# Performance work log

Measured on AMD Instinct MI355X. Metric: run time of the kernel, lower is better.

The kernel has to match this reference:

```python
import jax, jax.numpy as jnp
import numpy as np

B, T, C, HS = 64, 256, 2048, 128


def setup_inputs() -> dict:
    key = jax.random.key(0)
    k1, k2, k3, k4 = jax.random.split(key, 4)
    x = jax.random.normal(k1, (B, T, C), dtype=jnp.float32)
    # Dense(head_size, use_bias=False) kernels, scaled like glorot-ish init
    Wk = jax.random.normal(k2, (C, HS), dtype=jnp.float32) * (C ** -0.5)
    Wq = jax.random.normal(k3, (C, HS), dtype=jnp.float32) * (C ** -0.5)
    Wv = jax.random.normal(k4, (C, HS), dtype=jnp.float32) * (C ** -0.5)
    return {"x": x, "Wk": Wk, "Wq": Wq, "Wv": Wv}


def reference(x, Wk, Wq, Wv):
    Bn, Tn, Cn = x.shape
    k = jnp.einsum("btc,ch->bth", x, Wk)
    q = jnp.einsum("btc,ch->bth", x, Wq)
    v = jnp.einsum("btc,ch->bth", x, Wv)
    # faithful to source: scores = k @ q^T, scaled by C**-0.5 (input dim!)
    scores = jnp.einsum("bth,bsh->bts", k, q) * (Cn ** -0.5)
    causal = jnp.tril(jnp.ones((Tn, Tn), dtype=bool))  # [T, T]
    scores = jnp.where(causal, scores, -jnp.inf)
    weights = jax.nn.softmax(scores, axis=-1)
    return jnp.einsum("bts,bsh->bth", weights, v)
```

## Files before the change

kernel.cpp:

```cpp
#include <hip/hip_runtime.h>
#include <hip/hip_bf16.h>
#include <cstdint>
#include <cstddef>

#define B_  64
#define T_  256
#define C_  2048
#define HS_ 128
#define N_  384

typedef __bf16 bf16x8 __attribute__((ext_vector_type(8)));
typedef float  floatx4 __attribute__((ext_vector_type(4)));

__device__ __forceinline__ unsigned short f2bf_rne(float f) {
  union { float f; unsigned int u; } v; v.f = f;
  unsigned int r = v.u + 0x7fffu + ((v.u >> 16) & 1u);
  return (unsigned short)(r >> 16);
}
__device__ __forceinline__ unsigned short f2bf(float f) {
  union { float f; unsigned int u; } v; v.f = f;
  return (unsigned short)((v.u + 0x8000u) >> 16);
}

__device__ __forceinline__ void async_copy16(const void* g, void* l) {
  __builtin_amdgcn_global_load_lds(
      (const __attribute__((address_space(1))) unsigned int*)g,
      (__attribute__((address_space(3))) unsigned int*)l, 16, 0, 0);
}

__global__ __launch_bounds__(256) void wt_kernel(
    const float* __restrict__ Wk, const float* __restrict__ Wq,
    const float* __restrict__ Wv, unsigned short* __restrict__ Wt) {
  __shared__ float tile[32][33];
  const int w  = blockIdx.z;
  const int c0 = blockIdx.x * 32;
  const int h0 = blockIdx.y * 32;
  const float* W = (w == 0) ? Wk : (w == 1) ? Wq : Wv;
  const int tx = threadIdx.x & 31, ty = threadIdx.x >> 5;
#pragma unroll
  for (int i = 0; i < 32; i += 8)
    tile[ty + i][tx] = W[(size_t)(c0 + ty + i) * HS_ + h0 + tx];
  __syncthreads();
#pragma unroll
  for (int i = 0; i < 32; i += 8) {
    int hh = ty + i, cc = tx;
    Wt[(size_t)(w * HS_ + h0 + hh) * C_ + c0 + cc] = f2bf_rne(tile[cc][hh]);
  }
}

__global__ __launch_bounds__(256) void qkv_gemm(
    const float* __restrict__ X, const unsigned short* __restrict__ Wt,
    unsigned short* __restrict__ kqv, unsigned short* __restrict__ vT) {
  __shared__ unsigned short As[64 * 72];
  __shared__ unsigned short Bs[128 * 64];

  const int tid  = threadIdx.x;
  const int wave = tid >> 6, lane = tid & 63;
  const int quad = lane >> 4, l16 = lane & 15;

  const int g  = blockIdx.x;
  const int ml = g & 7, q8 = g >> 3;
  const int nb = q8 % 3, mh = q8 / 3;
  const int m0 = (mh * 8 + ml) * 64;
  const int n0 = nb * 128;
  const int wm = (wave >> 1) * 32;
  const int wn = (wave & 1) * 64;

  const int arow = tid >> 4;
  const int achk = tid & 15;

  floatx4 acc[2][4] = {};

  for (int k0 = 0; k0 < C_; k0 += 64) {
#pragma unroll
    for (int r = 0; r < 4; ++r) {
      int slot = (r * 4 + wave) * 64 + lane;
      int n = slot >> 3, sl = slot & 7;
      int c = sl ^ (n & 7);
      async_copy16(Wt + (size_t)(n0 + n) * C_ + k0 + c * 8,
                   &Bs[(size_t)((r * 4 + wave) * 64) * 8]);
    }
    float4 av[4];
#pragma unroll
    for (int r = 0; r < 4; ++r)
      av[r] = *(const float4*)(X + (size_t)(m0 + arow + r * 16) * C_ + k0 + achk * 4);
#pragma unroll
    for (int r = 0; r < 4; ++r) {
      ushort4 b4;
      b4.x = f2bf(av[r].x); b4.y = f2bf(av[r].y);
      b4.z = f2bf(av[r].z); b4.w = f2bf(av[r].w);
      *(ushort4*)&As[(arow + r * 16) * 72 + achk * 4] = b4;
    }
    __syncthreads();

#pragma unroll
    for (int ks = 0; ks < 2; ++ks) {
      bf16x8 af[2], bfv[4];
#pragma unroll
      for (int mt = 0; mt < 2; ++mt)
        af[mt] = *(const bf16x8*)&As[(wm + mt * 16 + l16) * 72 + ks * 32 + quad * 8];
#pragma unroll
      for (int nt = 0; nt < 4; ++nt) {
        int n = wn + nt * 16 + l16;
        int c = ks * 4 + quad;
        bfv[nt] = *(const bf16x8*)&Bs[n * 64 + (c ^ (n & 7)) * 8];
      }
#pragma unroll
      for (int mt = 0; mt < 2; ++mt)
#pragma unroll
        for (int nt = 0; nt < 4; ++nt)
          acc[mt][nt] = __builtin_amdgcn_mfma_f32_16x16x32_bf16(
              af[mt], bfv[nt], acc[mt][nt], 0, 0, 0);
    }
    __syncthreads();
  }

#pragma unroll
  for (int mt = 0; mt < 2; ++mt)
#pragma unroll
    for (int nt = 0; nt < 4; ++nt)
#pragma unroll
      for (int r = 0; r < 4; ++r) {
        int row = m0 + wm + mt * 16 + quad * 4 + r;
        int col = wn + nt * 16 + l16;
        unsigned short us = f2bf(acc[mt][nt][r]);
        kqv[(size_t)row * N_ + n0 + col] = us;
        if (n0 == 256) {
          int bb = row >> 8, tt = row & 255;
          vT[(size_t)bb * HS_ * T_ + (size_t)col * T_ + tt] = us;
        }
      }
}

__global__ __launch_bounds__(64) void attn_kernel(
    const unsigned short* __restrict__ kqv, const unsigned short* __restrict__ vT,
    float* __restrict__ out) {
  __shared__ unsigned short P[16 * 264];
  const int lane = threadIdx.x;
  const int quad = lane >> 4, l16 = lane & 15;
  const int tb = blockIdx.x;
  const int b  = blockIdx.y;
  const int t0 = tb * 16;
  const float scale = 0.022097086912079612f;
  const unsigned short* kq = kqv + (size_t)b * T_ * N_;

  bf16x8 kf[4];
#pragma unroll
  for (int ks = 0; ks < 4; ++ks)
    kf[ks] = *(const bf16x8*)&kq[(size_t)(t0 + l16) * N_ + ks * 32 + quad * 8];

  floatx4 S[16];
#pragma unroll
  for (int st = 0; st < 16; ++st) {
    if (st <= tb) {
      floatx4 a = {};
#pragma unroll
      for (int ks = 0; ks < 4; ++ks) {
        bf16x8 qf = *(const bf16x8*)&kq[(size_t)(st * 16 + l16) * N_ + HS_ +
                                        ks * 32 + quad * 8];
        a = __builtin_amdgcn_mfma_f32_16x16x32_bf16(kf[ks], qf, a, 0, 0, 0);
      }
      S[st] = a;
    }
  }

  float rsum[4] = {0.f, 0.f, 0.f, 0.f};
#pragma unroll
  for (int st = 0; st < 16; ++st) {
    if (st <= tb) {
      int scol = st * 16 + l16;
#pragma unroll
      for (int r = 0; r < 4; ++r) {
        int trow = t0 + quad * 4 + r;
        float p = (scol <= trow) ? __expf(S[st][r] * scale) : 0.f;
        S[st][r] = p;
        rsum[r] += p;
      }
    }
  }
#pragma unroll
  for (int m = 1; m < 16; m <<= 1)
#pragma unroll
    for (int r = 0; r < 4; ++r)
      rsum[r] += __shfl_xor(rsum[r], m, 64);

  const int st_hi = (tb + 2) & ~1;
#pragma unroll
  for (int st = 0; st < 16; ++st) {
    if (st < st_hi) {
#pragma unroll
      for (int r = 0; r < 4; ++r) {
        float p = (st <= tb) ? S[st][r] : 0.f;
        P[(quad * 4 + r) * 264 + st * 16 + l16] = f2bf(p);
      }
    }
  }
  __syncthreads();

  floatx4 oacc[8] = {};
  const unsigned short* vb = vT + (size_t)b * HS_ * T_;
  const int nks = (tb + 2) >> 1;
#pragma unroll
  for (int ks = 0; ks < 8; ++ks) {
    if (ks < nks) {
      bf16x8 pa = *(const bf16x8*)&P[l16 * 264 + ks * 32 + quad * 8];
#pragma unroll
      for (int nt = 0; nt < 8; ++nt) {
        bf16x8 bv = *(const bf16x8*)&vb[(size_t)(nt * 16 + l16) * T_ +
                                        ks * 32 + quad * 8];
        oacc[nt] = __builtin_amdgcn_mfma_f32_16x16x32_bf16(pa, bv, oacc[nt], 0, 0, 0);
      }
    }
  }

  float* ob = out + ((size_t)b * T_ + t0) * HS_;
#pragma unroll
  for (int nt = 0; nt < 8; ++nt)
#pragma unroll
    for (int r = 0; r < 4; ++r) {
      int row = quad * 4 + r;
      ob[(size_t)row * HS_ + nt * 16 + l16] = oacc[nt][r] / rsum[r];
    }
}

extern "C" void kernel_launch(void* const* d_in, const int* in_sizes, int n_in,
                              void* d_out, int out_size, void* d_ws, size_t ws_size,
                              hipStream_t stream) {
  const float* x  = (const float*)d_in[0];
  const float* Wk = (const float*)d_in[1];
  const float* Wq = (const float*)d_in[2];
  const float* Wv = (const float*)d_in[3];
  float* out = (float*)d_out;

  char* ws = (char*)d_ws;
  unsigned short* Wt  = (unsigned short*)(ws);
  unsigned short* kqv = (unsigned short*)(ws + 1572864);
  unsigned short* vT  = (unsigned short*)(ws + 1572864 + 12582912);

  hipLaunchKernelGGL(wt_kernel, dim3(64, 4, 3), dim3(256), 0, stream, Wk, Wq, Wv, Wt);
  hipLaunchKernelGGL(qkv_gemm, dim3(768), dim3(256), 0, stream, x, Wt, kqv, vT);
  hipLaunchKernelGGL(attn_kernel, dim3(16, 64), dim3(64), 0, stream, kqv, vT, out);
}
```

Before: 254.0 us.

## Double-buffer QKV GEMM loads and split attention keys across wave pairs

The QKV projection GEMM now double-buffers its shared-memory tiles and prefetches the next K-slice of weights and activations while computing the current one, which also removes one barrier per iteration. The attention kernel now runs four waves per block, covering two query tiles. Each pair of waves splits the causal key tiles by parity, software-prefetches Q and V fragments, and the two partial outputs and row sums are combined through shared memory. This targets exposed load latency in the GEMM and poor occupancy and load balance in attention, at the cost of more shared memory and registers plus an extra reduction step.

```diff
diff --git a/kernel.cpp b/kernel.cpp
--- a/kernel.cpp
+++ b/kernel.cpp
@@ -51,8 +51,8 @@
 __global__ __launch_bounds__(256) void qkv_gemm(
     const float* __restrict__ X, const unsigned short* __restrict__ Wt,
     unsigned short* __restrict__ kqv, unsigned short* __restrict__ vT) {
-  __shared__ unsigned short As[64 * 72];
-  __shared__ unsigned short Bs[128 * 64];
+  __shared__ unsigned short As[2][64 * 72];
+  __shared__ unsigned short Bs[2][128 * 64];
 
   const int tid  = threadIdx.x;
   const int wave = tid >> 6, lane = tid & 63;
@@ -69,41 +69,59 @@
   const int arow = tid >> 4;
   const int achk = tid & 15;
 
+  int bsrc_n[4], bsrc_c[4], bdst[4];
+#pragma unroll
+  for (int r = 0; r < 4; ++r) {
+    int slot = (r * 4 + wave) * 64 + lane;
+    int n = slot >> 3, sl = slot & 7;
+    bsrc_n[r] = n; bsrc_c[r] = sl ^ (n & 7);
+    bdst[r] = (r * 4 + wave) * 64 * 8;
+  }
+
+#pragma unroll
+  for (int r = 0; r < 4; ++r)
+    async_copy16(Wt + (size_t)(n0 + bsrc_n[r]) * C_ + bsrc_c[r] * 8,
+                 &Bs[0][bdst[r]]);
+  float4 av[4];
+#pragma unroll
+  for (int r = 0; r < 4; ++r)
+    av[r] = *(const float4*)(X + (size_t)(m0 + arow + r * 16) * C_ + achk * 4);
+
   floatx4 acc[2][4] = {};
 
-  for (int k0 = 0; k0 < C_; k0 += 64) {
-#pragma unroll
-    for (int r = 0; r < 4; ++r) {
-      int slot = (r * 4 + wave) * 64 + lane;
-      int n = slot >> 3, sl = slot & 7;
-      int c = sl ^ (n & 7);
-      async_copy16(Wt + (size_t)(n0 + n) * C_ + k0 + c * 8,
-                   &Bs[(size_t)((r * 4 + wave) * 64) * 8]);
-    }
-    float4 av[4];
-#pragma unroll
-    for (int r = 0; r < 4; ++r)
-      av[r] = *(const float4*)(X + (size_t)(m0 + arow + r * 16) * C_ + k0 + achk * 4);
+  for (int k = 0; k < 32; ++k) {
+    const int cur = k & 1, nxt = cur ^ 1;
 #pragma unroll
     for (int r = 0; r < 4; ++r) {
       ushort4 b4;
       b4.x = f2bf(av[r].x); b4.y = f2bf(av[r].y);
       b4.z = f2bf(av[r].z); b4.w = f2bf(av[r].w);
-      *(ushort4*)&As[(arow + r * 16) * 72 + achk * 4] = b4;
+      *(ushort4*)&As[cur][(arow + r * 16) * 72 + achk * 4] = b4;
     }
     __syncthreads();
+
+    if (k < 31) {
+      const int kn = (k + 1) * 64;
+#pragma unroll
+      for (int r = 0; r < 4; ++r)
+        async_copy16(Wt + (size_t)(n0 + bsrc_n[r]) * C_ + kn + bsrc_c[r] * 8,
+                     &Bs[nxt][bdst[r]]);
+#pragma unroll
+      for (int r = 0; r < 4; ++r)
+        av[r] = *(const float4*)(X + (size_t)(m0 + arow + r * 16) * C_ + kn + achk * 4);
+    }
 
 #pragma unroll
     for (int ks = 0; ks < 2; ++ks) {
       bf16x8 af[2], bfv[4];
 #pragma unroll
       for (int mt = 0; mt < 2; ++mt)
-        af[mt] = *(const bf16x8*)&As[(wm + mt * 16 + l16) * 72 + ks * 32 + quad * 8];
+        af[mt] = *(const bf16x8*)&As[cur][(wm + mt * 16 + l16) * 72 + ks * 32 + quad * 8];
 #pragma unroll
       for (int nt = 0; nt < 4; ++nt) {
         int n = wn + nt * 16 + l16;
         int c = ks * 4 + quad;
-        bfv[nt] = *(const bf16x8*)&Bs[n * 64 + (c ^ (n & 7)) * 8];
+        bfv[nt] = *(const bf16x8*)&Bs[cur][n * 64 + (c ^ (n & 7)) * 8];
       }
 #pragma unroll
       for (int mt = 0; mt < 2; ++mt)
@@ -112,7 +130,6 @@
           acc[mt][nt] = __builtin_amdgcn_mfma_f32_16x16x32_bf16(
               af[mt], bfv[nt], acc[mt][nt], 0, 0, 0);
     }
-    __syncthreads();
   }
 
 #pragma unroll
@@ -132,15 +149,20 @@
       }
 }
 
-__global__ __launch_bounds__(64) void attn_kernel(
+__global__ __launch_bounds__(256) void attn_kernel(
     const unsigned short* __restrict__ kqv, const unsigned short* __restrict__ vT,
     float* __restrict__ out) {
-  __shared__ unsigned short P[16 * 264];
-  const int lane = threadIdx.x;
+  __shared__ unsigned short P[4][16 * 136];
+  __shared__ float Olds[2][16][132];
+  __shared__ float rs1[2][16];
+
+  const int tid  = threadIdx.x;
+  const int wave = tid >> 6, lane = tid & 63;
   const int quad = lane >> 4, l16 = lane & 15;
-  const int tb = blockIdx.x;
+  const int tile = wave >> 1, par = wave & 1;
+  const int tt = blockIdx.x * 2 + tile;
   const int b  = blockIdx.y;
-  const int t0 = tb * 16;
+  const int t0 = tt * 16;
   const float scale = 0.022097086912079612f;
   const unsigned short* kq = kqv + (size_t)b * T_ * N_;
 
@@ -149,34 +171,46 @@
   for (int ks = 0; ks < 4; ++ks)
     kf[ks] = *(const bf16x8*)&kq[(size_t)(t0 + l16) * N_ + ks * 32 + quad * 8];
 
-  floatx4 S[16];
-#pragma unroll
-  for (int st = 0; st < 16; ++st) {
-    if (st <= tb) {
-      floatx4 a = {};
-#pragma unroll
-      for (int ks = 0; ks < 4; ++ks) {
-        bf16x8 qf = *(const bf16x8*)&kq[(size_t)(st * 16 + l16) * N_ + HS_ +
-                                        ks * 32 + quad * 8];
-        a = __builtin_amdgcn_mfma_f32_16x16x32_bf16(kf[ks], qf, a, 0, 0, 0);
-      }
-      S[st] = a;
-    }
-  }
+  const int n_my = ((tt + 1) + (1 - par)) >> 1;
+  const int npad = (n_my + 1) & ~1;
 
   float rsum[4] = {0.f, 0.f, 0.f, 0.f};
-#pragma unroll
-  for (int st = 0; st < 16; ++st) {
-    if (st <= tb) {
-      int scol = st * 16 + l16;
-#pragma unroll
-      for (int r = 0; r < 4; ++r) {
-        int trow = t0 + quad * 4 + r;
-        float p = (scol <= trow) ? __expf(S[st][r] * scale) : 0.f;
-        S[st][r] = p;
-        rsum[r] += p;
-      }
-    }
+
+  bf16x8 qf[4];
+  if (n_my > 0) {
+    const int st = par;
+#pragma unroll
+    for (int ks = 0; ks < 4; ++ks)
+      qf[ks] = *(const bf16x8*)&kq[(size_t)(st * 16 + l16) * N_ + HS_ + ks * 32 + quad * 8];
+  }
+  for (int j = 0; j < n_my; ++j) {
+    bf16x8 qn[4];
+    if (j + 1 < n_my) {
+      const int st = par + 2 * (j + 1);
+#pragma unroll
+      for (int ks = 0; ks < 4; ++ks)
+        qn[ks] = *(const bf16x8*)&kq[(size_t)(st * 16 + l16) * N_ + HS_ + ks * 32 + quad * 8];
+    }
+    floatx4 a = {};
+#pragma unroll
+    for (int ks = 0; ks < 4; ++ks)
+      a = __builtin_amdgcn_mfma_f32_16x16x32_bf16(kf[ks], qf[ks], a, 0, 0, 0);
+    const int st = par + 2 * j;
+    const int scol = st * 16 + l16;
+#pragma unroll
+    for (int r = 0; r < 4; ++r) {
+      int trow = t0 + quad * 4 + r;
+      float p = (scol <= trow) ? __expf(a[r] * scale) : 0.f;
+      rsum[r] += p;
+      P[wave][(quad * 4 + r) * 136 + j * 16 + l16] = f2bf(p);
+    }
+#pragma unroll
+    for (int ks = 0; ks < 4; ++ks) qf[ks] = qn[ks];
+  }
+  if (npad > n_my) {
+#pragma unroll
+    for (int r = 0; r < 4; ++r)
+      P[wave][(quad * 4 + r) * 136 + n_my * 16 + l16] = 0;
   }
 #pragma unroll
   for (int m = 1; m < 16; m <<= 1)
@@ -184,43 +218,66 @@
     for (int r = 0; r < 4; ++r)
       rsum[r] += __shfl_xor(rsum[r], m, 64);
 
-  const int st_hi = (tb + 2) & ~1;
-#pragma unroll
-  for (int st = 0; st < 16; ++st) {
-    if (st < st_hi) {
-#pragma unroll
-      for (int r = 0; r < 4; ++r) {
-        float p = (st <= tb) ? S[st][r] : 0.f;
-        P[(quad * 4 + r) * 264 + st * 16 + l16] = f2bf(p);
-      }
-    }
-  }
-  __syncthreads();
-
   floatx4 oacc[8] = {};
   const unsigned short* vb = vT + (size_t)b * HS_ * T_;
-  const int nks = (tb + 2) >> 1;
-#pragma unroll
-  for (int ks = 0; ks < 8; ++ks) {
-    if (ks < nks) {
-      bf16x8 pa = *(const bf16x8*)&P[l16 * 264 + ks * 32 + quad * 8];
-#pragma unroll
-      for (int nt = 0; nt < 8; ++nt) {
-        bf16x8 bv = *(const bf16x8*)&vb[(size_t)(nt * 16 + l16) * T_ +
-                                        ks * 32 + quad * 8];
-        oacc[nt] = __builtin_amdgcn_mfma_f32_16x16x32_bf16(pa, bv, oacc[nt], 0, 0, 0);
+  const int nks = npad >> 1;
+  const int sb_off = (quad >> 1);
+  const int sb_lo  = (quad & 1) * 8;
+  bf16x8 bv[8]; bf16x8 pa;
+  if (nks > 0) {
+    int st = par + 2 * (0 + sb_off);
+    int sbase = st * 16 + sb_lo;
+    pa = *(const bf16x8*)&P[wave][l16 * 136 + 0 * 32 + quad * 8];
+#pragma unroll
+    for (int nt = 0; nt < 8; ++nt)
+      bv[nt] = *(const bf16x8*)&vb[(size_t)(nt * 16 + l16) * T_ + sbase];
+  }
+  for (int ks2 = 0; ks2 < nks; ++ks2) {
+    bf16x8 bvn[8]; bf16x8 pan;
+    if (ks2 + 1 < nks) {
+      int jt = 2 * (ks2 + 1) + sb_off;
+      int st = par + 2 * jt;
+      int sbase = st * 16 + sb_lo;
+      pan = *(const bf16x8*)&P[wave][l16 * 136 + (ks2 + 1) * 32 + quad * 8];
+#pragma unroll
+      for (int nt = 0; nt < 8; ++nt)
+        bvn[nt] = *(const bf16x8*)&vb[(size_t)(nt * 16 + l16) * T_ + sbase];
+    }
+#pragma unroll
+    for (int nt = 0; nt < 8; ++nt)
+      oacc[nt] = __builtin_amdgcn_mfma_f32_16x16x32_bf16(pa, bv[nt], oacc[nt], 0, 0, 0);
+    pa = pan;
+#pragma unroll
+    for (int nt = 0; nt < 8; ++nt) bv[nt] = bvn[nt];
+  }
+
+  if (par == 1) {
+#pragma unroll
+    for (int nt = 0; nt < 8; ++nt)
+#pragma unroll
+      for (int r = 0; r < 4; ++r)
+        Olds[tile][quad * 4 + r][nt * 16 + l16] = oacc[nt][r];
+    if (l16 == 0) {
+#pragma unroll
+      for (int r = 0; r < 4; ++r) rs1[tile][quad * 4 + r] = rsum[r];
+    }
+  }
+  __syncthreads();
+  if (par == 0) {
+    float inv[4];
+#pragma unroll
+    for (int r = 0; r < 4; ++r)
+      inv[r] = 1.f / (rsum[r] + rs1[tile][quad * 4 + r]);
+    float* ob = out + ((size_t)b * T_ + t0) * HS_;
+#pragma unroll
+    for (int nt = 0; nt < 8; ++nt)
+#pragma unroll
+      for (int r = 0; r < 4; ++r) {
+        int row = quad * 4 + r;
+        ob[(size_t)row * HS_ + nt * 16 + l16] =
+            (oacc[nt][r] + Olds[tile][row][nt * 16 + l16]) * inv[r];
       }
-    }
-  }
-
-  float* ob = out + ((size_t)b * T_ + t0) * HS_;
-#pragma unroll
-  for (int nt = 0; nt < 8; ++nt)
-#pragma unroll
-    for (int r = 0; r < 4; ++r) {
-      int row = quad * 4 + r;
-      ob[(size_t)row * HS_ + nt * 16 + l16] = oacc[nt][r] / rsum[r];
-    }
+  }
 }
 
 extern "C" void kernel_launch(void* const* d_in, const int* in_sizes, int n_in,
@@ -239,5 +296,5 @@
 
   hipLaunchKernelGGL(wt_kernel, dim3(64, 4, 3), dim3(256), 0, stream, Wk, Wq, Wv, Wt);
   hipLaunchKernelGGL(qkv_gemm, dim3(768), dim3(256), 0, stream, x, Wt, kqv, vT);
-  hipLaunchKernelGGL(attn_kernel, dim3(16, 64), dim3(64), 0, stream, kqv, vT, out);
-}
+  hipLaunchKernelGGL(attn_kernel, dim3(8, 64), dim3(256), 0, stream, kqv, vT, out);
+}
```

Measured after the change: 244.2 us. -3.8%, faster.
